# Kernel optimization log

Hardware: AMD Instinct MI355X
Metric: run time of the kernel (lower is better)

The kernel has to match this reference:

```python
import jax, jax.numpy as jnp
import numpy as np

END_INDEX = 0
MAX_STEPS = 20
BEAM = 5
K = 5  # per_node_beam_size
VN = -1e20
B, S, V, H, D = 32, 4, 20000, 512, 2048


def setup_inputs() -> dict:
    key = jax.random.key(0)
    ks = jax.random.split(key, 7)
    image_feature = jax.random.normal(ks[0], (B, D), jnp.float32)
    start_predictions = jax.random.randint(ks[1], (B,), 0, V)
    state_transform = jax.random.bernoulli(ks[2], 0.9, (B, S, S, V))
    emb = jax.random.normal(ks[3], (V, H), jnp.float32) * 0.02
    W_h = jax.random.normal(ks[4], (H, H), jnp.float32) * 0.02
    W_im = jax.random.normal(ks[5], (D, H), jnp.float32) * 0.02
    W_out = jax.random.normal(ks[6], (H, V), jnp.float32) * 0.02
    return dict(image_feature=image_feature, start_predictions=start_predictions,
                state_transform=state_transform, emb=emb, W_h=W_h, W_im=W_im, W_out=W_out)


def _step(image_feat, tokens, h, emb, W_h, W_im, W_out):
    # minimal recurrent decoder standing in for the injected step_func
    h_new = jnp.tanh(emb[tokens] + h @ W_h + image_feat @ W_im)
    log_probs = jax.nn.log_softmax(h_new @ W_out, axis=-1)
    return log_probs, h_new


def reference(image_feature, start_predictions, state_transform, emb, W_h, W_im, W_out):
    mask_t = jnp.swapaxes(state_transform, 1, 2)  # [B, S_tgt, S_src, V]
    h0 = jnp.zeros((B, H), jnp.float32)
    lp0, h = _step(image_feature, start_predictions, h0, emb, W_h, W_im, W_out)  # [B,V]
    # initial masked topk from init_state=0: transitions 0 -> s
    state_pred = jnp.where(state_transform[:, 0], lp0[:, None, :], VN)  # [B,S,V]
    last_lp, pred0 = jax.lax.top_k(state_pred, BEAM)  # [B,S,BEAM]
    pred0_flat = pred0.reshape(B, S * BEAM)

    def enlarge(t):  # [B, ...] -> [B*S*BEAM, ...]
        return jnp.broadcast_to(t[:, None, None], (B, S, BEAM) + t.shape[1:]).reshape((B * S * BEAM,) + t.shape[1:])

    h = enlarge(h)
    img = enlarge(image_feature)
    after_end = jnp.full((V,), VN, jnp.float32).at[END_INDEX].set(0.0)

    def scan_step(carry, _):
        h, last_preds, last_lp = carry
        lp, h_new = _step(img, last_preds.reshape(-1), h, emb, W_h, W_im, W_out)  # [N,V]
        cleaned = jnp.where((last_preds.reshape(-1) == END_INDEX)[:, None], after_end, lp)
        cleaned = cleaned.reshape(B, S, BEAM, V)
        # masked scores over all target states at once: [B, S_tgt, S_src, BEAM, V]
        masked = jnp.where(mask_t[:, :, :, None, :], cleaned[:, None], VN)
        top_lp, top_cls = jax.lax.top_k(masked, K)  # [B,St,Ss,BEAM,K]
        summed = top_lp + last_lp[:, None, :, :, None]
        flat_lp = summed.reshape(B, S, S * BEAM * K)
        flat_cls = top_cls.reshape(B, S, S * BEAM * K)
        beam_lp, beam_idx = jax.lax.top_k(flat_lp, BEAM)  # [B,St,BEAM]
        pred = jnp.take_along_axis(flat_cls, beam_idx, axis=2)
        bp = (beam_idx // K).reshape(B, S * BEAM)  # backpointer into S_src*BEAM
        h_nxt = jnp.take_along_axis(h_new.reshape(B, S * BEAM, H), bp[:, :, None], axis=1).reshape(B * S * BEAM, H)
        preds_flat = pred.reshape(B, S * BEAM)
        return (h_nxt, preds_flat, beam_lp), (preds_flat, bp)

    (_, _, last_lp), (preds_seq, bps) = jax.lax.scan(
        scan_step, (h, pred0_flat, last_lp), None, length=MAX_STEPS - 1)
    predictions = jnp.concatenate([pred0_flat[None], preds_seq], 0)  # [T, B, S*BEAM]

    # backtrack through backpointers (reverse scan over time)
    def back_step(cur_bp, inp):
        preds_t, bp_prev = inp
        rec = jnp.take_along_axis(preds_t, cur_bp, axis=1)
        return jnp.take_along_axis(bp_prev, cur_bp, axis=1), rec

    cur_bp, rec_mid = jax.lax.scan(back_step, bps[-1], (predictions[1:-1], bps[:-1]), reverse=True)
    rec0 = jnp.take_along_axis(predictions[0], cur_bp, axis=1)
    all_preds = jnp.concatenate([rec0[None], rec_mid, predictions[-1][None]], 0)  # [T,B,S*BEAM]
    all_predictions = jnp.moveaxis(all_preds, 0, 2).reshape(B, S, BEAM, MAX_STEPS)
    # select_state_func is user-injected; identity selection: return beams + scores
    return all_predictions, last_lp
```

## Files before the change

### kernel.cpp

```cpp
#include <hip/hip_runtime.h>
#include <hip/hip_bf16.h>
#include <stdint.h>
#include <stddef.h>

namespace {

constexpr int CB = 32;
constexpr int CS = 4;
constexpr int CV = 20000;
constexpr int CH = 512;
constexpr int CBEAM = 5;
constexpr int CT = 20;
constexpr int CNR = CB * CS * CBEAM;
constexpr int CSB = CS * CBEAM;
constexpr int CNM = CB * CS * CS * CV;
constexpr int CNP = CB * CS * CV;
constexpr float VNF = -1e20f;
constexpr float NEGINF = -3.402823466e+38f;
constexpr int IMAX = 0x7fffffff;

__global__ void detect_mode_k(const unsigned int* __restrict__ w, int* __restrict__ mode) {
  if (threadIdx.x != 0 || blockIdx.x != 0) return;
  int all01 = 1, odd1 = 0, f1 = 0;
  for (int i = 0; i < 256; ++i) {
    unsigned int x = w[i];
    if (x > 1u) all01 = 0;
    if ((i & 1) && x == 1u) odd1++;
    if (x == 0x3f800000u) f1++;
  }
  int md;
  if (f1 > 128) md = 3;
  else if (all01) md = (odd1 > 8) ? 1 : 2;
  else md = 0;
  *mode = md;
}

__global__ void convert_pack_k(const void* __restrict__ st, unsigned char* __restrict__ pm,
                               const int* __restrict__ mode) {
  int md = *mode;
  for (int i = blockIdx.x * blockDim.x + threadIdx.x; i < CNP; i += gridDim.x * blockDim.x) {
    int v = i % CV;
    int bs = i / CV;
    size_t base = (size_t)bs * 4 * CV + v;
    unsigned char r = 0;
#pragma unroll
    for (int s = 0; s < 4; ++s) {
      size_t idx = base + (size_t)s * CV;
      unsigned char bit;
      if (md == 0)      bit = ((const unsigned char*)st)[idx] != 0;
      else if (md == 1) bit = ((const unsigned int*)st)[idx] != 0;
      else if (md == 2) bit = ((const unsigned int*)st)[2 * idx] != 0;
      else              bit = (((const unsigned int*)st)[idx] & 0x7fffffffu) != 0;
      r |= (unsigned char)(bit << s);
    }
    pm[i] = r;
  }
}

__global__ __launch_bounds__(256) void img_proj_k(const float* __restrict__ img,
                                                  const float* __restrict__ Wim,
                                                  float* __restrict__ out) {
  int b = blockIdx.x, tid = threadIdx.x;
  __shared__ float simg[2048];
  for (int i = tid; i < 2048; i += 256) simg[i] = img[b * 2048 + i];
  __syncthreads();
  int c0 = tid * 2;
  float a0 = 0.f, a1 = 0.f;
  for (int k = 0; k < 2048; ++k) {
    float x = simg[k];
    float2 w = *(const float2*)&Wim[(size_t)k * CH + c0];
    a0 = fmaf(x, w.x, a0);
    a1 = fmaf(x, w.y, a1);
  }
  out[b * CH + c0] = a0;
  out[b * CH + c0 + 1] = a1;
}

__global__ void init_h_k(const float* __restrict__ emb, const int* __restrict__ start,
                         const float* __restrict__ imgp, float* __restrict__ H0) {
  int b = blockIdx.x, tid = threadIdx.x;
  int tok = start[b];
  for (int c = tid; c < CH; c += 256)
    H0[b * CH + c] = tanhf(emb[(size_t)tok * CH + c] + imgp[b * CH + c]);
}

template <int BM, int BN, int KB, int MT, int NT, int EPI>
__global__ __launch_bounds__(256) void gemm_k(
    const float* __restrict__ A, const int* __restrict__ rowmap,
    const float* __restrict__ Bm, float* __restrict__ C,
    int M, int N, int K,
    const int* __restrict__ tok, const float* __restrict__ emb,
    const float* __restrict__ imgp) {
  constexpr int TX = BN / NT;
  constexpr int TY = BM / MT;
  static_assert(TX * TY == 256, "thread count");
  static_assert((BM * KB / 4) % 256 == 0 && (KB * BN / 4) % 256 == 0, "stage");
  __shared__ float As[KB][BM + 4];
  __shared__ float Bs[KB][BN + 4];
  const int bm = blockIdx.y * BM;
  const int bn = blockIdx.x * BN;
  const int tid = threadIdx.x;
  const int tx = tid % TX, ty = tid / TX;
  float acc[MT][NT];
#pragma unroll
  for (int i = 0; i < MT; ++i)
#pragma unroll
    for (int j = 0; j < NT; ++j) acc[i][j] = 0.f;

  for (int k0 = 0; k0 < K; k0 += KB) {
    constexpr int AIT = BM * KB / 4 / 256;
#pragma unroll
    for (int it = 0; it < AIT; ++it) {
      int i = tid + it * 256;
      int r = i / (KB / 4);
      int kq = i % (KB / 4);
      int row = bm + r;
      float4 v = make_float4(0.f, 0.f, 0.f, 0.f);
      if (row < M) {
        int sr = rowmap ? rowmap[row] : row;
        v = *(const float4*)&A[(size_t)sr * K + k0 + kq * 4];
      }
      As[kq * 4 + 0][r] = v.x;
      As[kq * 4 + 1][r] = v.y;
      As[kq * 4 + 2][r] = v.z;
      As[kq * 4 + 3][r] = v.w;
    }
    constexpr int BIT = KB * BN / 4 / 256;
#pragma unroll
    for (int it = 0; it < BIT; ++it) {
      int i = tid + it * 256;
      int kk = i / (BN / 4);
      int cq = i % (BN / 4);
      int col = bn + cq * 4;
      float4 v = make_float4(0.f, 0.f, 0.f, 0.f);
      if (col < N) v = *(const float4*)&Bm[(size_t)(k0 + kk) * N + col];
      *(float4*)&Bs[kk][cq * 4] = v;
    }
    __syncthreads();
#pragma unroll 8
    for (int kk = 0; kk < KB; ++kk) {
      float a[MT], bb[NT];
#pragma unroll
      for (int i = 0; i < MT; ++i) a[i] = As[kk][ty * MT + i];
#pragma unroll
      for (int j = 0; j < NT; ++j) bb[j] = Bs[kk][tx * NT + j];
#pragma unroll
      for (int i = 0; i < MT; ++i)
#pragma unroll
        for (int j = 0; j < NT; ++j) acc[i][j] = fmaf(a[i], bb[j], acc[i][j]);
    }
    __syncthreads();
  }
#pragma unroll
  for (int i = 0; i < MT; ++i) {
    int row = bm + ty * MT + i;
    if (row < M) {
#pragma unroll
      for (int j4 = 0; j4 < NT / 4; ++j4) {
        int col = bn + tx * NT + j4 * 4;
        if (col < N) {
          float4 v;
          v.x = acc[i][j4 * 4 + 0];
          v.y = acc[i][j4 * 4 + 1];
          v.z = acc[i][j4 * 4 + 2];
          v.w = acc[i][j4 * 4 + 3];
          if (EPI == 1) {
            size_t eb = (size_t)tok[row] * N;
            int ib = (row / CSB) * N;
            v.x = tanhf(v.x + emb[eb + col + 0] + imgp[ib + col + 0]);
            v.y = tanhf(v.y + emb[eb + col + 1] + imgp[ib + col + 1]);
            v.z = tanhf(v.z + emb[eb + col + 2] + imgp[ib + col + 2]);
            v.w = tanhf(v.w + emb[eb + col + 3] + imgp[ib + col + 3]);
          }
          *(float4*)&C[(size_t)row * N + col] = v;
        }
      }
    }
  }
}

__global__ __launch_bounds__(256) void lse_k(const float* __restrict__ logits,
                                             float* __restrict__ lse) {
  int row = blockIdx.x;
  int tid = threadIdx.x;
  const float* lp = logits + (size_t)row * CV;
  __shared__ float red[4];
  float m = NEGINF;
  for (int v = tid * 4; v < CV; v += 1024) {
    float4 x = *(const float4*)(lp + v);
    m = fmaxf(m, fmaxf(fmaxf(x.x, x.y), fmaxf(x.z, x.w)));
  }
#pragma unroll
  for (int off = 32; off > 0; off >>= 1) m = fmaxf(m, __shfl_xor(m, off));
  if ((tid & 63) == 0) red[tid >> 6] = m;
  __syncthreads();
  m = fmaxf(fmaxf(red[0], red[1]), fmaxf(red[2], red[3]));
  __syncthreads();
  float s = 0.f;
  for (int v = tid * 4; v < CV; v += 1024) {
    float4 x = *(const float4*)(lp + v);
    s += expf(x.x - m) + expf(x.y - m) + expf(x.z - m) + expf(x.w - m);
  }
#pragma unroll
  for (int off = 32; off > 0; off >>= 1) s += __shfl_xor(s, off);
  if ((tid & 63) == 0) red[tid >> 6] = s;
  __syncthreads();
  if (tid == 0) lse[row] = m + logf(red[0] + red[1] + red[2] + red[3]);
}

struct L5 {
  float v0, v1, v2, v3, v4;
  int i0, i1, i2, i3, i4;
};

__device__ __forceinline__ void initL(L5& l) {
  l.v0 = l.v1 = l.v2 = l.v3 = l.v4 = NEGINF;
  l.i0 = l.i1 = l.i2 = l.i3 = l.i4 = IMAX;
}

__device__ __forceinline__ void insL(L5& l, float val, int idx) {
  if (!(val > l.v4)) return;
  if (val > l.v0) {
    l.v4 = l.v3; l.i4 = l.i3; l.v3 = l.v2; l.i3 = l.i2; l.v2 = l.v1; l.i2 = l.i1;
    l.v1 = l.v0; l.i1 = l.i0; l.v0 = val; l.i0 = idx;
  } else if (val > l.v1) {
    l.v4 = l.v3; l.i4 = l.i3; l.v3 = l.v2; l.i3 = l.i2; l.v2 = l.v1; l.i2 = l.i1;
    l.v1 = val; l.i1 = idx;
  } else if (val > l.v2) {
    l.v4 = l.v3; l.i4 = l.i3; l.v3 = l.v2; l.i3 = l.i2; l.v2 = val; l.i2 = idx;
  } else if (val > l.v3) {
    l.v4 = l.v3; l.i4 = l.i3; l.v3 = val; l.i3 = idx;
  } else {
    l.v4 = val; l.i4 = idx;
  }
}

__device__ __forceinline__ void mergeL(L5& A, L5 B) {
  float o0, o1, o2, o3, o4;
  int q0, q1, q2, q3, q4;
#define MSTEP(OV, OI)                                                                    \
  {                                                                                      \
    bool ta = (A.v0 > B.v0) || (A.v0 == B.v0 && A.i0 < B.i0);                            \
    if (ta) {                                                                            \
      OV = A.v0; OI = A.i0;                                                              \
      A.v0 = A.v1; A.i0 = A.i1; A.v1 = A.v2; A.i1 = A.i2; A.v2 = A.v3; A.i2 = A.i3;      \
      A.v3 = A.v4; A.i3 = A.i4; A.v4 = NEGINF; A.i4 = IMAX;                              \
    } else {                                                                             \
      OV = B.v0; OI = B.i0;                                                              \
      B.v0 = B.v1; B.i0 = B.i1; B.v1 = B.v2; B.i1 = B.i2; B.v2 = B.v3; B.i2 = B.i3;      \
      B.v3 = B.v4; B.i3 = B.i4; B.v4 = NEGINF; B.i4 = IMAX;                              \
    }                                                                                    \
  }
  MSTEP(o0, q0) MSTEP(o1, q1) MSTEP(o2, q2) MSTEP(o3, q3) MSTEP(o4, q4)
#undef MSTEP
  A.v0 = o0; A.v1 = o1; A.v2 = o2; A.v3 = o3; A.v4 = o4;
  A.i0 = q0; A.i1 = q1; A.i2 = q2; A.i3 = q3; A.i4 = q4;
}

__device__ __forceinline__ L5 shflxL(const L5& a, int off) {
  L5 r;
  r.v0 = __shfl_xor(a.v0, off); r.v1 = __shfl_xor(a.v1, off); r.v2 = __shfl_xor(a.v2, off);
  r.v3 = __shfl_xor(a.v3, off); r.v4 = __shfl_xor(a.v4, off);
  r.i0 = __shfl_xor(a.i0, off); r.i1 = __shfl_xor(a.i1, off); r.i2 = __shfl_xor(a.i2, off);
  r.i3 = __shfl_xor(a.i3, off); r.i4 = __shfl_xor(a.i4, off);
  return r;
}

template <bool INIT>
__global__ __launch_bounds__(256) void topk_half_k(
    const float* __restrict__ logits, const float* __restrict__ lse,
    const unsigned char* __restrict__ pmask, const int* __restrict__ last_preds,
    float* __restrict__ hv_lp, int* __restrict__ hv_cls) {
  constexpr int HV = CV / 2;
  constexpr int NG = HV / 4;
  int blk = blockIdx.x;
  int half = blk & 1, row = blk >> 1;
  int b, ss;
  if (INIT) { b = row; ss = 0; }
  else { b = row / CSB; ss = (row / CBEAM) % CS; }
  const int tid = threadIdx.x;
  const unsigned char* prow = pmask + (size_t)(b * CS + ss) * CV;

  if (!INIT && last_preds[row] == 0) {
    if (tid == 0) {
      unsigned char m0 = prow[0];
#pragma unroll
      for (int st = 0; st < 4; ++st) {
        int base = ((row * 4 + st) * 2 + half) * 5;
        if (half == 0) {
          hv_lp[base] = ((m0 >> st) & 1) ? 0.0f : VNF;
          hv_cls[base] = 0;
#pragma unroll
          for (int k = 1; k < 5; ++k) { hv_lp[base + k] = VNF; hv_cls[base + k] = k; }
        } else {
#pragma unroll
          for (int k = 0; k < 5; ++k) { hv_lp[base + k] = VNF; hv_cls[base + k] = HV + k; }
        }
      }
    }
    return;
  }

  const float* lprow = logits + (size_t)row * CV + (size_t)half * HV;
  const unsigned char* ph = prow + (size_t)half * HV;
  float lsev = lse[row];

  L5 lst0, lst1, lst2, lst3;
  initL(lst0); initL(lst1); initL(lst2); initL(lst3);

#define PROC1(VAL, IDX, BITS)                 \
  {                                           \
    if ((BITS) & 1) insL(lst0, VAL, IDX);     \
    if ((BITS) & 2) insL(lst1, VAL, IDX);     \
    if ((BITS) & 4) insL(lst2, VAL, IDX);     \
    if ((BITS) & 8) insL(lst3, VAL, IDX);     \
  }
#define PROC4(X, M, G)                                                        \
  {                                                                           \
    int ibase = half * HV + (G) * 4;                                          \
    float s0 = (X).x - lsev, s1 = (X).y - lsev;                               \
    float s2 = (X).z - lsev, s3 = (X).w - lsev;                               \
    PROC1(s0, ibase + 0, (M))                                                 \
    PROC1(s1, ibase + 1, (M) >> 8)                                            \
    PROC1(s2, ibase + 2, (M) >> 16)                                           \
    PROC1(s3, ibase + 3, (M) >> 24)                                           \
  }

  for (int g = tid; g < NG; g += 512) {
    int g2 = g + 256;
    float4 x0 = *(const float4*)(lprow + (size_t)g * 4);
    unsigned int m0 = *(const unsigned int*)(ph + (size_t)g * 4);
    float4 x1 = make_float4(0.f, 0.f, 0.f, 0.f);
    unsigned int m1 = 0;
    bool has1 = (g2 < NG);
    if (has1) {
      x1 = *(const float4*)(lprow + (size_t)g2 * 4);
      m1 = *(const unsigned int*)(ph + (size_t)g2 * 4);
    }
    PROC4(x0, m0, g)
    if (has1) PROC4(x1, m1, g2)
  }
#undef PROC4
#undef PROC1

#pragma unroll
  for (int off = 1; off < 64; off <<= 1) {
    mergeL(lst0, shflxL(lst0, off));
    mergeL(lst1, shflxL(lst1, off));
    mergeL(lst2, shflxL(lst2, off));
    mergeL(lst3, shflxL(lst3, off));
  }

  __shared__ float swv[4][4][5];
  __shared__ int swi[4][4][5];
  int wid = tid >> 6, lane = tid & 63;
  if (lane == 0) {
#define POST(L, ST)                                                     \
    swv[wid][ST][0] = L.v0; swv[wid][ST][1] = L.v1; swv[wid][ST][2] = L.v2; \
    swv[wid][ST][3] = L.v3; swv[wid][ST][4] = L.v4;                     \
    swi[wid][ST][0] = L.i0; swi[wid][ST][1] = L.i1; swi[wid][ST][2] = L.i2; \
    swi[wid][ST][3] = L.i3; swi[wid][ST][4] = L.i4;
    POST(lst0, 0) POST(lst1, 1) POST(lst2, 2) POST(lst3, 3)
#undef POST
  }
  __syncthreads();
  if (tid == 0) {
#pragma unroll
    for (int st = 0; st < 4; ++st) {
      L5 A;
      A.v0 = swv[0][st][0]; A.v1 = swv[0][st][1]; A.v2 = swv[0][st][2];
      A.v3 = swv[0][st][3]; A.v4 = swv[0][st][4];
      A.i0 = swi[0][st][0]; A.i1 = swi[0][st][1]; A.i2 = swi[0][st][2];
      A.i3 = swi[0][st][3]; A.i4 = swi[0][st][4];
#pragma unroll
      for (int w = 1; w < 4; ++w) {
        L5 Bb;
        Bb.v0 = swv[w][st][0]; Bb.v1 = swv[w][st][1]; Bb.v2 = swv[w][st][2];
        Bb.v3 = swv[w][st][3]; Bb.v4 = swv[w][st][4];
        Bb.i0 = swi[w][st][0]; Bb.i1 = swi[w][st][1]; Bb.i2 = swi[w][st][2];
        Bb.i3 = swi[w][st][3]; Bb.i4 = swi[w][st][4];
        mergeL(A, Bb);
      }
      int base = ((row * 4 + st) * 2 + half) * 5;
      hv_lp[base + 0] = A.v0; hv_lp[base + 1] = A.v1; hv_lp[base + 2] = A.v2;
      hv_lp[base + 3] = A.v3; hv_lp[base + 4] = A.v4;
      hv_cls[base + 0] = A.i0; hv_cls[base + 1] = A.i1; hv_cls[base + 2] = A.i2;
      hv_cls[base + 3] = A.i3; hv_cls[base + 4] = A.i4;
    }
  }
}

template <bool INIT>
__global__ void merge_halves_k(const float* __restrict__ hv_lp, const int* __restrict__ hv_cls,
                               float* __restrict__ top_lp, int* __restrict__ top_cls,
                               float* __restrict__ lp0, int* __restrict__ preds0,
                               int* __restrict__ lastp_out, int* __restrict__ rowmap) {
  int gid = blockIdx.x * blockDim.x + threadIdx.x;
  int nit = (INIT ? CB : CNR) * 4;
  if (gid >= nit) return;
  int row = gid / 4, st = gid % 4;
  const float* a = hv_lp + (size_t)gid * 10;
  const int* ai = hv_cls + (size_t)gid * 10;
  L5 A, Bb;
  A.v0 = a[0]; A.v1 = a[1]; A.v2 = a[2]; A.v3 = a[3]; A.v4 = a[4];
  A.i0 = ai[0]; A.i1 = ai[1]; A.i2 = ai[2]; A.i3 = ai[3]; A.i4 = ai[4];
  Bb.v0 = a[5]; Bb.v1 = a[6]; Bb.v2 = a[7]; Bb.v3 = a[8]; Bb.v4 = a[9];
  Bb.i0 = ai[5]; Bb.i1 = ai[6]; Bb.i2 = ai[7]; Bb.i3 = ai[8]; Bb.i4 = ai[9];
  mergeL(A, Bb);
  if (INIT) {
    int slot = row * CSB + st * 5;
    float vv[5] = {A.v0, A.v1, A.v2, A.v3, A.v4};
    int ii[5] = {A.i0, A.i1, A.i2, A.i3, A.i4};
#pragma unroll
    for (int k = 0; k < 5; ++k) {
      lp0[slot + k] = vv[k];
      preds0[slot + k] = ii[k];
      lastp_out[slot + k] = ii[k];
      rowmap[slot + k] = row;
    }
  } else {
    int b = row / CSB, ss = (row / CBEAM) % CS, beam = row % CBEAM;
    int o = (((b * CS + st) * CS + ss) * CBEAM + beam) * 5;
    top_lp[o + 0] = A.v0; top_lp[o + 1] = A.v1; top_lp[o + 2] = A.v2;
    top_lp[o + 3] = A.v3; top_lp[o + 4] = A.v4;
    top_cls[o + 0] = A.i0; top_cls[o + 1] = A.i1; top_cls[o + 2] = A.i2;
    top_cls[o + 3] = A.i3; top_cls[o + 4] = A.i4;
  }
}

__global__ __launch_bounds__(128) void beam_sel_k(
    const float* __restrict__ top_lp, const int* __restrict__ top_cls,
    const float* __restrict__ lp_old, float* __restrict__ lp_new,
    int* __restrict__ last_preds, int* __restrict__ rowmap,
    int* __restrict__ preds_t, int* __restrict__ bps_t) {
  int b = blockIdx.x / CS, st = blockIdx.x % CS;
  int tid = threadIdx.x;
  __shared__ float sv[128];
  __shared__ int si[128];
  float val = NEGINF;
  int idx = IMAX;
  if (tid < 100) {
    int ss = tid / 25, rem = tid % 25;
    int beam = rem / 5, k = rem % 5;
    val = top_lp[(size_t)(((b * CS + st) * CS + ss) * CBEAM + beam) * 5 + k] +
          lp_old[(b * CS + ss) * CBEAM + beam];
    idx = tid;
  }
  for (int r = 0; r < 5; ++r) {
    sv[tid] = val;
    si[tid] = idx;
    __syncthreads();
    for (int off = 64; off > 0; off >>= 1) {
      if (tid < off) {
        float w = sv[tid + off];
        int wi = si[tid + off];
        if (w > sv[tid] || (w == sv[tid] && wi < si[tid])) { sv[tid] = w; si[tid] = wi; }
      }
      __syncthreads();
    }
    float wval = sv[0];
    int widx = si[0];
    if (idx == widx) { val = NEGINF; idx = IMAX; }
    if (tid == r) {
      int ss = widx / 25, rem = widx % 25;
      int beam = rem / 5, k = rem % 5;
      int pred = top_cls[(size_t)(((b * CS + st) * CS + ss) * CBEAM + beam) * 5 + k];
      int bp = widx / 5;
      int slot = (b * CS + st) * CBEAM + r;
      lp_new[slot] = wval;
      preds_t[slot] = pred;
      bps_t[slot] = bp;
      last_preds[slot] = pred;
      rowmap[slot] = b * CSB + bp;
    }
    __syncthreads();
  }
}

__global__ void backtrack_k(const int* __restrict__ preds, const int* __restrict__ bps,
                            const float* __restrict__ lpfin, float* __restrict__ out) {
  int b = blockIdx.x, j = threadIdx.x;
  if (j >= CSB) return;
  int s = j / CBEAM, bm = j % CBEAM;
  int obase = ((b * CS + s) * CBEAM + bm) * CT;
  int tok = preds[(CT - 1) * CNR + b * CSB + j];
  out[obase + CT - 1] = (float)tok;
  int cur = bps[(CT - 2) * CNR + b * CSB + j];
  for (int t = CT - 2; t >= 1; --t) {
    tok = preds[t * CNR + b * CSB + cur];
    out[obase + t] = (float)tok;
    cur = bps[(t - 1) * CNR + b * CSB + cur];
  }
  tok = preds[0 * CNR + b * CSB + cur];
  out[obase + 0] = (float)tok;
  out[CB * CS * CBEAM * CT + b * CSB + j] = lpfin[b * CSB + j];
}

}

extern "C" void kernel_launch(void* const* d_in, const int* in_sizes, int n_in,
                              void* d_out, int out_size, void* d_ws, size_t ws_size,
                              hipStream_t stream) {
  (void)in_sizes; (void)n_in; (void)out_size; (void)ws_size;
  const float* img = (const float*)d_in[0];
  const int* startp = (const int*)d_in[1];
  const void* straw = d_in[2];
  const float* emb = (const float*)d_in[3];
  const float* Wh = (const float*)d_in[4];
  const float* Wim = (const float*)d_in[5];
  const float* Wout = (const float*)d_in[6];
  float* out = (float*)d_out;

  char* ws = (char*)d_ws;
  size_t off = 0;
  auto take = [&](size_t bytes) -> char* {
    char* p = ws + off;
    off += (bytes + 255) & ~(size_t)255;
    return p;
  };
  unsigned char* pmask = (unsigned char*)take((size_t)CNP);
  int* modep = (int*)take(256);
  float* imgproj = (float*)take((size_t)CB * CH * 4);
  float* H0 = (float*)take((size_t)CNR * CH * 4);
  float* H1 = (float*)take((size_t)CNR * CH * 4);
  float* logits = (float*)take((size_t)CNR * CV * 4);
  float* lsebuf = (float*)take((size_t)CNR * 4);
  float* LP0 = (float*)take((size_t)CNR * 4);
  float* LP1 = (float*)take((size_t)CNR * 4);
  int* lastp = (int*)take((size_t)CNR * 4);
  int* rowmap = (int*)take((size_t)CNR * 4);
  float* toplp = (float*)take((size_t)2560 * 5 * 4);
  int* topcls = (int*)take((size_t)2560 * 5 * 4);
  float* hvlp = (float*)take((size_t)CNR * 4 * 2 * 5 * 4);
  int* hvcls = (int*)take((size_t)CNR * 4 * 2 * 5 * 4);
  int* predsq = (int*)take((size_t)CT * CNR * 4);
  int* bpsq = (int*)take((size_t)(CT - 1) * CNR * 4);

  detect_mode_k<<<1, 64, 0, stream>>>((const unsigned int*)straw, modep);
  convert_pack_k<<<1024, 256, 0, stream>>>(straw, pmask, modep);
  img_proj_k<<<CB, 256, 0, stream>>>(img, Wim, imgproj);
  init_h_k<<<CB, 256, 0, stream>>>(emb, startp, imgproj, H0);
  gemm_k<128, 128, 32, 8, 8, 0><<<dim3(157, 1), 256, 0, stream>>>(
      H0, nullptr, Wout, logits, CB, CV, CH, nullptr, nullptr, nullptr);
  lse_k<<<CB, 256, 0, stream>>>(logits, lsebuf);
  topk_half_k<true><<<CB * 2, 256, 0, stream>>>(logits, lsebuf, pmask, nullptr, hvlp, hvcls);
  merge_halves_k<true><<<1, 128, 0, stream>>>(hvlp, hvcls, nullptr, nullptr, LP0, predsq,
                                              lastp, rowmap);
  for (int t = 1; t < CT; ++t) {
    float* hprev = (t & 1) ? H0 : H1;
    float* hcur = (t & 1) ? H1 : H0;
    float* lpold = (t & 1) ? LP0 : LP1;
    float* lpnew = (t & 1) ? LP1 : LP0;
    gemm_k<32, 64, 32, 2, 4, 1><<<dim3(8, 20), 256, 0, stream>>>(
        hprev, rowmap, Wh, hcur, CNR, CH, CH, lastp, emb, imgproj);
    gemm_k<128, 128, 32, 8, 8, 0><<<dim3(157, 5), 256, 0, stream>>>(
        hcur, nullptr, Wout, logits, CNR, CV, CH, nullptr, nullptr, nullptr);
    lse_k<<<CNR, 256, 0, stream>>>(logits, lsebuf);
    topk_half_k<false><<<CNR * 2, 256, 0, stream>>>(logits, lsebuf, pmask, lastp, hvlp, hvcls);
    merge_halves_k<false><<<10, 256, 0, stream>>>(hvlp, hvcls, toplp, topcls, nullptr,
                                                  nullptr, nullptr, nullptr);
    beam_sel_k<<<CB * CS, 128, 0, stream>>>(toplp, topcls, lpold, lpnew, lastp, rowmap,
                                            predsq + (size_t)t * CNR,
                                            bpsq + (size_t)(t - 1) * CNR);
  }
  backtrack_k<<<CB, 32, 0, stream>>>(predsq, bpsq, LP1, out);
}
```

Before: 6.675 ms.

## Fuse output GEMM with log-softmax and masked top-k using split-fp16 MFMA

Replaces the fp32 SIMT output projection, the separate log-sum-exp pass and the top-k passes with one fused kernel per step. It uses fp16 matrix-core instructions with a hi/lo split of both operands (three MFMAs per tile) to approximate fp32 accuracy. Each tile computes partial online max/sum and a masked top-5 per state in registers, so the full 640x20000 logits matrix is never written to or reread from global memory. A small reduce kernel then merges the per-tile partials. The costs are a one-time transpose and split of W_out, scaled split arithmetic that could perturb ties and ordering, and more partial-merge work.

```diff
diff --git a/kernel.cpp b/kernel.cpp
--- a/kernel.cpp
+++ b/kernel.cpp
@@ -5,19 +5,31 @@
 
 namespace {
 
+typedef _Float16 f16;
+typedef __attribute__((ext_vector_type(8))) _Float16 f16x8;
+typedef __attribute__((ext_vector_type(4))) _Float16 f16x4;
+typedef __attribute__((ext_vector_type(4))) float f32x4;
+
 constexpr int CB = 32;
 constexpr int CS = 4;
 constexpr int CV = 20000;
+constexpr int CVP = 20224;
+constexpr int NTILE = 79;
 constexpr int CH = 512;
 constexpr int CBEAM = 5;
 constexpr int CT = 20;
 constexpr int CNR = CB * CS * CBEAM;
 constexpr int CSB = CS * CBEAM;
-constexpr int CNM = CB * CS * CS * CV;
 constexpr int CNP = CB * CS * CV;
 constexpr float VNF = -1e20f;
 constexpr float NEGINF = -3.402823466e+38f;
 constexpr int IMAX = 0x7fffffff;
+
+__device__ __forceinline__ void f2h2(float x, f16& h, f16& l) {
+  float xs = x * 256.0f;
+  h = (f16)xs;
+  l = (f16)(xs - (float)h);
+}
 
 __global__ void detect_mode_k(const unsigned int* __restrict__ w, int* __restrict__ mode) {
   if (threadIdx.x != 0 || blockIdx.x != 0) return;
@@ -54,6 +66,32 @@
       r |= (unsigned char)(bit << s);
     }
     pm[i] = r;
+  }
+}
+
+__global__ __launch_bounds__(256) void conv_wout_k(const float* __restrict__ W,
+                                                   f16* __restrict__ BTh,
+                                                   f16* __restrict__ BTl) {
+  __shared__ float t[64][65];
+  int n0 = blockIdx.x * 64, k0 = blockIdx.y * 64;
+  int tid = threadIdx.x;
+  int c = tid & 63, r4 = tid >> 6;
+#pragma unroll
+  for (int i = 0; i < 16; ++i) {
+    int kr = r4 + i * 4;
+    int n = n0 + c;
+    t[kr][c] = (n < CV) ? W[(size_t)(k0 + kr) * CV + n] : 0.f;
+  }
+  __syncthreads();
+#pragma unroll
+  for (int i = 0; i < 16; ++i) {
+    int nr = r4 + i * 4;
+    float x = t[c][nr];
+    f16 h, l;
+    f2h2(x, h, l);
+    size_t o = (size_t)(n0 + nr) * CH + k0 + c;
+    BTh[o] = h;
+    BTl[o] = l;
   }
 }
 
@@ -77,24 +115,30 @@
 }
 
 __global__ void init_h_k(const float* __restrict__ emb, const int* __restrict__ start,
-                         const float* __restrict__ imgp, float* __restrict__ H0) {
+                         const float* __restrict__ imgp, float* __restrict__ H0,
+                         f16* __restrict__ Hh, f16* __restrict__ Hl) {
   int b = blockIdx.x, tid = threadIdx.x;
   int tok = start[b];
-  for (int c = tid; c < CH; c += 256)
-    H0[b * CH + c] = tanhf(emb[(size_t)tok * CH + c] + imgp[b * CH + c]);
-}
-
-template <int BM, int BN, int KB, int MT, int NT, int EPI>
+  for (int c = tid; c < CH; c += 256) {
+    float v = tanhf(emb[(size_t)tok * CH + c] + imgp[b * CH + c]);
+    H0[b * CH + c] = v;
+    f16 h, l;
+    f2h2(v, h, l);
+    Hh[b * CH + c] = h;
+    Hl[b * CH + c] = l;
+  }
+}
+
+template <int BM, int BN, int KB, int MT, int NT>
 __global__ __launch_bounds__(256) void gemm_k(
     const float* __restrict__ A, const int* __restrict__ rowmap,
     const float* __restrict__ Bm, float* __restrict__ C,
     int M, int N, int K,
     const int* __restrict__ tok, const float* __restrict__ emb,
-    const float* __restrict__ imgp) {
+    const float* __restrict__ imgp, f16* __restrict__ Hh, f16* __restrict__ Hl) {
   constexpr int TX = BN / NT;
   constexpr int TY = BM / MT;
   static_assert(TX * TY == 256, "thread count");
-  static_assert((BM * KB / 4) % 256 == 0 && (KB * BN / 4) % 256 == 0, "stage");
   __shared__ float As[KB][BM + 4];
   __shared__ float Bs[KB][BN + 4];
   const int bm = blockIdx.y * BM;
@@ -164,48 +208,26 @@
           v.y = acc[i][j4 * 4 + 1];
           v.z = acc[i][j4 * 4 + 2];
           v.w = acc[i][j4 * 4 + 3];
-          if (EPI == 1) {
-            size_t eb = (size_t)tok[row] * N;
-            int ib = (row / CSB) * N;
-            v.x = tanhf(v.x + emb[eb + col + 0] + imgp[ib + col + 0]);
-            v.y = tanhf(v.y + emb[eb + col + 1] + imgp[ib + col + 1]);
-            v.z = tanhf(v.z + emb[eb + col + 2] + imgp[ib + col + 2]);
-            v.w = tanhf(v.w + emb[eb + col + 3] + imgp[ib + col + 3]);
-          }
+          size_t eb = (size_t)tok[row] * N;
+          int ib = (row / CSB) * N;
+          v.x = tanhf(v.x + emb[eb + col + 0] + imgp[ib + col + 0]);
+          v.y = tanhf(v.y + emb[eb + col + 1] + imgp[ib + col + 1]);
+          v.z = tanhf(v.z + emb[eb + col + 2] + imgp[ib + col + 2]);
+          v.w = tanhf(v.w + emb[eb + col + 3] + imgp[ib + col + 3]);
           *(float4*)&C[(size_t)row * N + col] = v;
+          f16 h0, h1, h2, h3, l0, l1, l2, l3;
+          f2h2(v.x, h0, l0);
+          f2h2(v.y, h1, l1);
+          f2h2(v.z, h2, l2);
+          f2h2(v.w, h3, l3);
+          f16x4 hv = {h0, h1, h2, h3};
+          f16x4 lv = {l0, l1, l2, l3};
+          *(f16x4*)&Hh[(size_t)row * N + col] = hv;
+          *(f16x4*)&Hl[(size_t)row * N + col] = lv;
         }
       }
     }
   }
-}
-
-__global__ __launch_bounds__(256) void lse_k(const float* __restrict__ logits,
-                                             float* __restrict__ lse) {
-  int row = blockIdx.x;
-  int tid = threadIdx.x;
-  const float* lp = logits + (size_t)row * CV;
-  __shared__ float red[4];
-  float m = NEGINF;
-  for (int v = tid * 4; v < CV; v += 1024) {
-    float4 x = *(const float4*)(lp + v);
-    m = fmaxf(m, fmaxf(fmaxf(x.x, x.y), fmaxf(x.z, x.w)));
-  }
-#pragma unroll
-  for (int off = 32; off > 0; off >>= 1) m = fmaxf(m, __shfl_xor(m, off));
-  if ((tid & 63) == 0) red[tid >> 6] = m;
-  __syncthreads();
-  m = fmaxf(fmaxf(red[0], red[1]), fmaxf(red[2], red[3]));
-  __syncthreads();
-  float s = 0.f;
-  for (int v = tid * 4; v < CV; v += 1024) {
-    float4 x = *(const float4*)(lp + v);
-    s += expf(x.x - m) + expf(x.y - m) + expf(x.z - m) + expf(x.w - m);
-  }
-#pragma unroll
-  for (int off = 32; off > 0; off >>= 1) s += __shfl_xor(s, off);
-  if ((tid & 63) == 0) red[tid >> 6] = s;
-  __syncthreads();
-  if (tid == 0) lse[row] = m + logf(red[0] + red[1] + red[2] + red[3]);
 }
 
 struct L5 {
@@ -267,169 +289,261 @@
 }
 
 template <bool INIT>
-__global__ __launch_bounds__(256) void topk_half_k(
-    const float* __restrict__ logits, const float* __restrict__ lse,
-    const unsigned char* __restrict__ pmask, const int* __restrict__ last_preds,
-    float* __restrict__ hv_lp, int* __restrict__ hv_cls) {
-  constexpr int HV = CV / 2;
-  constexpr int NG = HV / 4;
-  int blk = blockIdx.x;
-  int half = blk & 1, row = blk >> 1;
-  int b, ss;
-  if (INIT) { b = row; ss = 0; }
-  else { b = row / CSB; ss = (row / CBEAM) % CS; }
+__global__ __launch_bounds__(256) void fused_gemm_k(
+    const f16* __restrict__ Ah, const f16* __restrict__ Al,
+    const f16* __restrict__ BTh, const f16* __restrict__ BTl,
+    const unsigned char* __restrict__ pmask,
+    float* __restrict__ pv, unsigned short* __restrict__ pi, float* __restrict__ pms) {
+  const int tile = blockIdx.x;
+  const int bty = blockIdx.y * 64;
   const int tid = threadIdx.x;
-  const unsigned char* prow = pmask + (size_t)(b * CS + ss) * CV;
-
-  if (!INIT && last_preds[row] == 0) {
-    if (tid == 0) {
-      unsigned char m0 = prow[0];
-#pragma unroll
-      for (int st = 0; st < 4; ++st) {
-        int base = ((row * 4 + st) * 2 + half) * 5;
-        if (half == 0) {
-          hv_lp[base] = ((m0 >> st) & 1) ? 0.0f : VNF;
-          hv_cls[base] = 0;
-#pragma unroll
-          for (int k = 1; k < 5; ++k) { hv_lp[base + k] = VNF; hv_cls[base + k] = k; }
-        } else {
-#pragma unroll
-          for (int k = 0; k < 5; ++k) { hv_lp[base + k] = VNF; hv_cls[base + k] = HV + k; }
+  const int w = tid >> 6;
+  const int lane = tid & 63;
+  const int l16 = lane & 15, lq = lane >> 4;
+  const int vwave = tile * 256 + w * 64;
+
+  const f16* pvh = BTh + (size_t)(vwave + l16) * CH + lq * 8;
+  const f16* pvl = BTl + (size_t)(vwave + l16) * CH + lq * 8;
+  const f16* pbh = Ah + (size_t)(bty + l16) * CH + lq * 8;
+  const f16* pbl = Al + (size_t)(bty + l16) * CH + lq * 8;
+
+  f32x4 acc[4][4] = {};
+  for (int k0 = 0; k0 < CH; k0 += 32) {
+    f16x8 vh[4], vl[4], bh[4], bl[4];
+#pragma unroll
+    for (int i = 0; i < 4; ++i) {
+      vh[i] = *(const f16x8*)(pvh + (size_t)i * 16 * CH + k0);
+      vl[i] = *(const f16x8*)(pvl + (size_t)i * 16 * CH + k0);
+      bh[i] = *(const f16x8*)(pbh + (size_t)i * 16 * CH + k0);
+      bl[i] = *(const f16x8*)(pbl + (size_t)i * 16 * CH + k0);
+    }
+#pragma unroll
+    for (int vf = 0; vf < 4; ++vf)
+#pragma unroll
+      for (int bt = 0; bt < 4; ++bt) {
+        acc[vf][bt] = __builtin_amdgcn_mfma_f32_16x16x32_f16(vh[vf], bh[bt], acc[vf][bt], 0, 0, 0);
+        acc[vf][bt] = __builtin_amdgcn_mfma_f32_16x16x32_f16(vh[vf], bl[bt], acc[vf][bt], 0, 0, 0);
+        acc[vf][bt] = __builtin_amdgcn_mfma_f32_16x16x32_f16(vl[vf], bh[bt], acc[vf][bt], 0, 0, 0);
+      }
+  }
+
+  __shared__ float lv[4][64][4][5];
+  __shared__ unsigned short li[4][64][4][5];
+  __shared__ float lms[4][64][2];
+
+#pragma unroll
+  for (int bt = 0; bt < 4; ++bt) {
+    const int btrow = bty + bt * 16 + l16;
+    int mrow;
+    if (INIT) mrow = min(btrow, CB - 1) * CS;
+    else {
+      int b = btrow / CSB;
+      int ss = (btrow % CSB) / CBEAM;
+      mrow = b * CS + ss;
+    }
+    const unsigned char* pmrow = pmask + (size_t)mrow * CV;
+    float xv[4][4];
+    unsigned int msk[4];
+    float mloc = NEGINF;
+#pragma unroll
+    for (int vf = 0; vf < 4; ++vf) {
+      int cb = vwave + vf * 16 + lq * 4;
+      msk[vf] = *(const unsigned int*)(pmrow + cb);
+#pragma unroll
+      for (int rr = 0; rr < 4; ++rr) {
+        float x = acc[vf][bt][rr] * (1.0f / 65536.0f);
+        bool ok = (cb + rr) < CV;
+        xv[vf][rr] = ok ? x : NEGINF;
+        if (ok) mloc = fmaxf(mloc, x);
+      }
+    }
+    float sloc = 0.f;
+    L5 ls0, ls1, ls2, ls3;
+    initL(ls0); initL(ls1); initL(ls2); initL(ls3);
+#pragma unroll
+    for (int vf = 0; vf < 4; ++vf) {
+      int cb = vwave + vf * 16 + lq * 4;
+#pragma unroll
+      for (int rr = 0; rr < 4; ++rr) {
+        int col = cb + rr;
+        if (col < CV) {
+          float x = xv[vf][rr];
+          sloc += expf(x - mloc);
+          unsigned int bits = msk[vf] >> (rr * 8);
+          if (bits & 1u) insL(ls0, x, col);
+          if (bits & 2u) insL(ls1, x, col);
+          if (bits & 4u) insL(ls2, x, col);
+          if (bits & 8u) insL(ls3, x, col);
         }
       }
     }
-    return;
-  }
-
-  const float* lprow = logits + (size_t)row * CV + (size_t)half * HV;
-  const unsigned char* ph = prow + (size_t)half * HV;
-  float lsev = lse[row];
-
-  L5 lst0, lst1, lst2, lst3;
-  initL(lst0); initL(lst1); initL(lst2); initL(lst3);
-
-#define PROC1(VAL, IDX, BITS)                 \
-  {                                           \
-    if ((BITS) & 1) insL(lst0, VAL, IDX);     \
-    if ((BITS) & 2) insL(lst1, VAL, IDX);     \
-    if ((BITS) & 4) insL(lst2, VAL, IDX);     \
-    if ((BITS) & 8) insL(lst3, VAL, IDX);     \
-  }
-#define PROC4(X, M, G)                                                        \
-  {                                                                           \
-    int ibase = half * HV + (G) * 4;                                          \
-    float s0 = (X).x - lsev, s1 = (X).y - lsev;                               \
-    float s2 = (X).z - lsev, s3 = (X).w - lsev;                               \
-    PROC1(s0, ibase + 0, (M))                                                 \
-    PROC1(s1, ibase + 1, (M) >> 8)                                            \
-    PROC1(s2, ibase + 2, (M) >> 16)                                           \
-    PROC1(s3, ibase + 3, (M) >> 24)                                           \
-  }
-
-  for (int g = tid; g < NG; g += 512) {
-    int g2 = g + 256;
-    float4 x0 = *(const float4*)(lprow + (size_t)g * 4);
-    unsigned int m0 = *(const unsigned int*)(ph + (size_t)g * 4);
-    float4 x1 = make_float4(0.f, 0.f, 0.f, 0.f);
-    unsigned int m1 = 0;
-    bool has1 = (g2 < NG);
-    if (has1) {
-      x1 = *(const float4*)(lprow + (size_t)g2 * 4);
-      m1 = *(const unsigned int*)(ph + (size_t)g2 * 4);
-    }
-    PROC4(x0, m0, g)
-    if (has1) PROC4(x1, m1, g2)
-  }
-#undef PROC4
-#undef PROC1
-
-#pragma unroll
-  for (int off = 1; off < 64; off <<= 1) {
-    mergeL(lst0, shflxL(lst0, off));
-    mergeL(lst1, shflxL(lst1, off));
-    mergeL(lst2, shflxL(lst2, off));
-    mergeL(lst3, shflxL(lst3, off));
-  }
-
-  __shared__ float swv[4][4][5];
-  __shared__ int swi[4][4][5];
-  int wid = tid >> 6, lane = tid & 63;
-  if (lane == 0) {
-#define POST(L, ST)                                                     \
-    swv[wid][ST][0] = L.v0; swv[wid][ST][1] = L.v1; swv[wid][ST][2] = L.v2; \
-    swv[wid][ST][3] = L.v3; swv[wid][ST][4] = L.v4;                     \
-    swi[wid][ST][0] = L.i0; swi[wid][ST][1] = L.i1; swi[wid][ST][2] = L.i2; \
-    swi[wid][ST][3] = L.i3; swi[wid][ST][4] = L.i4;
-    POST(lst0, 0) POST(lst1, 1) POST(lst2, 2) POST(lst3, 3)
-#undef POST
+#pragma unroll
+    for (int off = 16; off <= 32; off <<= 1) {
+      mergeL(ls0, shflxL(ls0, off));
+      mergeL(ls1, shflxL(ls1, off));
+      mergeL(ls2, shflxL(ls2, off));
+      mergeL(ls3, shflxL(ls3, off));
+      float m2 = __shfl_xor(mloc, off);
+      float s2 = __shfl_xor(sloc, off);
+      float mn = fmaxf(mloc, m2);
+      sloc = sloc * expf(mloc - mn) + s2 * expf(m2 - mn);
+      mloc = mn;
+    }
+    if (lq == 0) {
+      int lrow = bt * 16 + l16;
+#define PUT(L, ST)                                                                      \
+      lv[w][lrow][ST][0] = L.v0; lv[w][lrow][ST][1] = L.v1; lv[w][lrow][ST][2] = L.v2;  \
+      lv[w][lrow][ST][3] = L.v3; lv[w][lrow][ST][4] = L.v4;                             \
+      li[w][lrow][ST][0] = (unsigned short)L.i0; li[w][lrow][ST][1] = (unsigned short)L.i1; \
+      li[w][lrow][ST][2] = (unsigned short)L.i2; li[w][lrow][ST][3] = (unsigned short)L.i3; \
+      li[w][lrow][ST][4] = (unsigned short)L.i4;
+      PUT(ls0, 0) PUT(ls1, 1) PUT(ls2, 2) PUT(ls3, 3)
+#undef PUT
+      lms[w][lrow][0] = mloc;
+      lms[w][lrow][1] = sloc;
+    }
   }
   __syncthreads();
-  if (tid == 0) {
-#pragma unroll
-    for (int st = 0; st < 4; ++st) {
-      L5 A;
-      A.v0 = swv[0][st][0]; A.v1 = swv[0][st][1]; A.v2 = swv[0][st][2];
-      A.v3 = swv[0][st][3]; A.v4 = swv[0][st][4];
-      A.i0 = swi[0][st][0]; A.i1 = swi[0][st][1]; A.i2 = swi[0][st][2];
-      A.i3 = swi[0][st][3]; A.i4 = swi[0][st][4];
-#pragma unroll
-      for (int w = 1; w < 4; ++w) {
-        L5 Bb;
-        Bb.v0 = swv[w][st][0]; Bb.v1 = swv[w][st][1]; Bb.v2 = swv[w][st][2];
-        Bb.v3 = swv[w][st][3]; Bb.v4 = swv[w][st][4];
-        Bb.i0 = swi[w][st][0]; Bb.i1 = swi[w][st][1]; Bb.i2 = swi[w][st][2];
-        Bb.i3 = swi[w][st][3]; Bb.i4 = swi[w][st][4];
-        mergeL(A, Bb);
-      }
-      int base = ((row * 4 + st) * 2 + half) * 5;
-      hv_lp[base + 0] = A.v0; hv_lp[base + 1] = A.v1; hv_lp[base + 2] = A.v2;
-      hv_lp[base + 3] = A.v3; hv_lp[base + 4] = A.v4;
-      hv_cls[base + 0] = A.i0; hv_cls[base + 1] = A.i1; hv_cls[base + 2] = A.i2;
-      hv_cls[base + 3] = A.i3; hv_cls[base + 4] = A.i4;
+
+  {
+    int row64 = tid >> 2, st = tid & 3;
+    L5 A;
+    A.v0 = lv[0][row64][st][0]; A.v1 = lv[0][row64][st][1]; A.v2 = lv[0][row64][st][2];
+    A.v3 = lv[0][row64][st][3]; A.v4 = lv[0][row64][st][4];
+    A.i0 = li[0][row64][st][0]; A.i1 = li[0][row64][st][1]; A.i2 = li[0][row64][st][2];
+    A.i3 = li[0][row64][st][3]; A.i4 = li[0][row64][st][4];
+#pragma unroll
+    for (int ww = 1; ww < 4; ++ww) {
+      L5 B;
+      B.v0 = lv[ww][row64][st][0]; B.v1 = lv[ww][row64][st][1]; B.v2 = lv[ww][row64][st][2];
+      B.v3 = lv[ww][row64][st][3]; B.v4 = lv[ww][row64][st][4];
+      B.i0 = li[ww][row64][st][0]; B.i1 = li[ww][row64][st][1]; B.i2 = li[ww][row64][st][2];
+      B.i3 = li[ww][row64][st][3]; B.i4 = li[ww][row64][st][4];
+      mergeL(A, B);
+    }
+    int grow = bty + row64;
+    size_t pbase = ((size_t)tile * CNR + grow) * 20 + st * 5;
+    pv[pbase + 0] = A.v0; pv[pbase + 1] = A.v1; pv[pbase + 2] = A.v2;
+    pv[pbase + 3] = A.v3; pv[pbase + 4] = A.v4;
+    pi[pbase + 0] = (unsigned short)A.i0; pi[pbase + 1] = (unsigned short)A.i1;
+    pi[pbase + 2] = (unsigned short)A.i2; pi[pbase + 3] = (unsigned short)A.i3;
+    pi[pbase + 4] = (unsigned short)A.i4;
+    if (st == 0) {
+      float m = lms[0][row64][0], s = lms[0][row64][1];
+#pragma unroll
+      for (int ww = 1; ww < 4; ++ww) {
+        float m2 = lms[ww][row64][0], s2 = lms[ww][row64][1];
+        float mn = fmaxf(m, m2);
+        s = s * expf(m - mn) + s2 * expf(m2 - mn);
+        m = mn;
+      }
+      pms[((size_t)tile * CNR + grow) * 2 + 0] = m;
+      pms[((size_t)tile * CNR + grow) * 2 + 1] = s;
     }
   }
 }
 
 template <bool INIT>
-__global__ void merge_halves_k(const float* __restrict__ hv_lp, const int* __restrict__ hv_cls,
-                               float* __restrict__ top_lp, int* __restrict__ top_cls,
-                               float* __restrict__ lp0, int* __restrict__ preds0,
-                               int* __restrict__ lastp_out, int* __restrict__ rowmap) {
-  int gid = blockIdx.x * blockDim.x + threadIdx.x;
-  int nit = (INIT ? CB : CNR) * 4;
-  if (gid >= nit) return;
-  int row = gid / 4, st = gid % 4;
-  const float* a = hv_lp + (size_t)gid * 10;
-  const int* ai = hv_cls + (size_t)gid * 10;
-  L5 A, Bb;
-  A.v0 = a[0]; A.v1 = a[1]; A.v2 = a[2]; A.v3 = a[3]; A.v4 = a[4];
-  A.i0 = ai[0]; A.i1 = ai[1]; A.i2 = ai[2]; A.i3 = ai[3]; A.i4 = ai[4];
-  Bb.v0 = a[5]; Bb.v1 = a[6]; Bb.v2 = a[7]; Bb.v3 = a[8]; Bb.v4 = a[9];
-  Bb.i0 = ai[5]; Bb.i1 = ai[6]; Bb.i2 = ai[7]; Bb.i3 = ai[8]; Bb.i4 = ai[9];
-  mergeL(A, Bb);
-  if (INIT) {
-    int slot = row * CSB + st * 5;
-    float vv[5] = {A.v0, A.v1, A.v2, A.v3, A.v4};
-    int ii[5] = {A.i0, A.i1, A.i2, A.i3, A.i4};
-#pragma unroll
-    for (int k = 0; k < 5; ++k) {
-      lp0[slot + k] = vv[k];
-      preds0[slot + k] = ii[k];
-      lastp_out[slot + k] = ii[k];
-      rowmap[slot + k] = row;
-    }
-  } else {
-    int b = row / CSB, ss = (row / CBEAM) % CS, beam = row % CBEAM;
-    int o = (((b * CS + st) * CS + ss) * CBEAM + beam) * 5;
-    top_lp[o + 0] = A.v0; top_lp[o + 1] = A.v1; top_lp[o + 2] = A.v2;
-    top_lp[o + 3] = A.v3; top_lp[o + 4] = A.v4;
-    top_cls[o + 0] = A.i0; top_cls[o + 1] = A.i1; top_cls[o + 2] = A.i2;
-    top_cls[o + 3] = A.i3; top_cls[o + 4] = A.i4;
+__global__ __launch_bounds__(64) void reduce_k(
+    const float* __restrict__ pv, const unsigned short* __restrict__ pi,
+    const float* __restrict__ pms, const unsigned char* __restrict__ pmask,
+    const int* __restrict__ lastp_in,
+    float* __restrict__ fin_v, int* __restrict__ fin_i, float* __restrict__ lsebuf,
+    float* __restrict__ lp0, int* __restrict__ preds0,
+    int* __restrict__ lastp_out, int* __restrict__ rowmap) {
+  int row = blockIdx.x;
+  int t = threadIdx.x;
+  int st = t >> 4, c = t & 15;
+  L5 A;
+  initL(A);
+  float m = NEGINF, s = 0.f;
+  for (int j = 0; j < 5; ++j) {
+    int tl = c * 5 + j;
+    if (tl >= NTILE) break;
+    size_t base = ((size_t)tl * CNR + row) * 20 + st * 5;
+    L5 B;
+    B.v0 = pv[base + 0]; B.v1 = pv[base + 1]; B.v2 = pv[base + 2];
+    B.v3 = pv[base + 3]; B.v4 = pv[base + 4];
+    B.i0 = pi[base + 0]; B.i1 = pi[base + 1]; B.i2 = pi[base + 2];
+    B.i3 = pi[base + 3]; B.i4 = pi[base + 4];
+    mergeL(A, B);
+    if (st == 0) {
+      float mt = pms[((size_t)tl * CNR + row) * 2 + 0];
+      float stv = pms[((size_t)tl * CNR + row) * 2 + 1];
+      float mn = fmaxf(m, mt);
+      s = s * expf(m - mn) + stv * expf(mt - mn);
+      m = mn;
+    }
+  }
+  __shared__ float shv[4][16][5];
+  __shared__ int shi[4][16][5];
+  __shared__ float shm[16], shs[16];
+  __shared__ float shlse;
+  shv[st][c][0] = A.v0; shv[st][c][1] = A.v1; shv[st][c][2] = A.v2;
+  shv[st][c][3] = A.v3; shv[st][c][4] = A.v4;
+  shi[st][c][0] = A.i0; shi[st][c][1] = A.i1; shi[st][c][2] = A.i2;
+  shi[st][c][3] = A.i3; shi[st][c][4] = A.i4;
+  if (st == 0) { shm[c] = m; shs[c] = s; }
+  for (int off = 8; off >= 1; off >>= 1) {
+    __syncthreads();
+    if (c < off) {
+      L5 B;
+      B.v0 = shv[st][c + off][0]; B.v1 = shv[st][c + off][1]; B.v2 = shv[st][c + off][2];
+      B.v3 = shv[st][c + off][3]; B.v4 = shv[st][c + off][4];
+      B.i0 = shi[st][c + off][0]; B.i1 = shi[st][c + off][1]; B.i2 = shi[st][c + off][2];
+      B.i3 = shi[st][c + off][3]; B.i4 = shi[st][c + off][4];
+      mergeL(A, B);
+      shv[st][c][0] = A.v0; shv[st][c][1] = A.v1; shv[st][c][2] = A.v2;
+      shv[st][c][3] = A.v3; shv[st][c][4] = A.v4;
+      shi[st][c][0] = A.i0; shi[st][c][1] = A.i1; shi[st][c][2] = A.i2;
+      shi[st][c][3] = A.i3; shi[st][c][4] = A.i4;
+      if (st == 0) {
+        float m2 = shm[c + off], s2 = shs[c + off];
+        float mn = fmaxf(m, m2);
+        s = s * expf(m - mn) + s2 * expf(m2 - mn);
+        m = mn;
+        shm[c] = m; shs[c] = s;
+      }
+    }
+  }
+  __syncthreads();
+  if (t == 0) shlse = shm[0] + logf(shs[0]);
+  __syncthreads();
+  float lse = shlse;
+  if (c == 0) {
+    if (INIT) {
+      float vv[5] = {A.v0, A.v1, A.v2, A.v3, A.v4};
+      int ii[5] = {A.i0, A.i1, A.i2, A.i3, A.i4};
+      int slot = row * CSB + st * 5;
+#pragma unroll
+      for (int k = 0; k < 5; ++k) {
+        lp0[slot + k] = vv[k] - lse;
+        preds0[slot + k] = ii[k];
+        lastp_out[slot + k] = ii[k];
+        rowmap[slot + k] = row;
+      }
+    } else {
+      bool ended = (lastp_in[row] == 0);
+      if (ended) {
+        int b = row / CSB, ss = (row % CSB) / CBEAM;
+        unsigned char mb = pmask[(size_t)(b * CS + ss) * CV];
+        A.v0 = ((mb >> st) & 1) ? 0.0f : VNF; A.i0 = 0;
+        A.v1 = VNF; A.i1 = 1; A.v2 = VNF; A.i2 = 2;
+        A.v3 = VNF; A.i3 = 3; A.v4 = VNF; A.i4 = 4;
+      }
+      size_t fb = ((size_t)row * 4 + st) * 5;
+      fin_v[fb + 0] = A.v0; fin_v[fb + 1] = A.v1; fin_v[fb + 2] = A.v2;
+      fin_v[fb + 3] = A.v3; fin_v[fb + 4] = A.v4;
+      fin_i[fb + 0] = A.i0; fin_i[fb + 1] = A.i1; fin_i[fb + 2] = A.i2;
+      fin_i[fb + 3] = A.i3; fin_i[fb + 4] = A.i4;
+      if (st == 0) lsebuf[row] = ended ? 0.f : lse;
+    }
   }
 }
 
 __global__ __launch_bounds__(128) void beam_sel_k(
-    const float* __restrict__ top_lp, const int* __restrict__ top_cls,
+    const float* __restrict__ fin_v, const int* __restrict__ fin_i,
+    const float* __restrict__ lsebuf,
     const float* __restrict__ lp_old, float* __restrict__ lp_new,
     int* __restrict__ last_preds, int* __restrict__ rowmap,
     int* __restrict__ preds_t, int* __restrict__ bps_t) {
@@ -440,10 +554,9 @@
   float val = NEGINF;
   int idx = IMAX;
   if (tid < 100) {
-    int ss = tid / 25, rem = tid % 25;
-    int beam = rem / 5, k = rem % 5;
-    val = top_lp[(size_t)(((b * CS + st) * CS + ss) * CBEAM + beam) * 5 + k] +
-          lp_old[(b * CS + ss) * CBEAM + beam];
+    int r5 = tid / 5, k = tid % 5;
+    int row = b * CSB + r5;
+    val = fin_v[((size_t)row * 4 + st) * 5 + k] - lsebuf[row] + lp_old[row];
     idx = tid;
   }
   for (int r = 0; r < 5; ++r) {
@@ -462,10 +575,10 @@
     int widx = si[0];
     if (idx == widx) { val = NEGINF; idx = IMAX; }
     if (tid == r) {
-      int ss = widx / 25, rem = widx % 25;
-      int beam = rem / 5, k = rem % 5;
-      int pred = top_cls[(size_t)(((b * CS + st) * CS + ss) * CBEAM + beam) * 5 + k];
-      int bp = widx / 5;
+      int r5 = widx / 5, k = widx % 5;
+      int row = b * CSB + r5;
+      int pred = fin_i[((size_t)row * 4 + st) * 5 + k];
+      int bp = r5;
       int slot = (b * CS + st) * CBEAM + r;
       lp_new[slot] = wval;
       preds_t[slot] = pred;
@@ -518,48 +631,48 @@
     off += (bytes + 255) & ~(size_t)255;
     return p;
   };
-  unsigned char* pmask = (unsigned char*)take((size_t)CNP);
+  unsigned char* pmask = (unsigned char*)take((size_t)CNP + 512);
   int* modep = (int*)take(256);
   float* imgproj = (float*)take((size_t)CB * CH * 4);
   float* H0 = (float*)take((size_t)CNR * CH * 4);
   float* H1 = (float*)take((size_t)CNR * CH * 4);
-  float* logits = (float*)take((size_t)CNR * CV * 4);
   float* lsebuf = (float*)take((size_t)CNR * 4);
   float* LP0 = (float*)take((size_t)CNR * 4);
   float* LP1 = (float*)take((size_t)CNR * 4);
   int* lastp = (int*)take((size_t)CNR * 4);
   int* rowmap = (int*)take((size_t)CNR * 4);
-  float* toplp = (float*)take((size_t)2560 * 5 * 4);
-  int* topcls = (int*)take((size_t)2560 * 5 * 4);
-  float* hvlp = (float*)take((size_t)CNR * 4 * 2 * 5 * 4);
-  int* hvcls = (int*)take((size_t)CNR * 4 * 2 * 5 * 4);
   int* predsq = (int*)take((size_t)CT * CNR * 4);
   int* bpsq = (int*)take((size_t)(CT - 1) * CNR * 4);
+  f16* BTh = (f16*)take((size_t)CVP * CH * 2);
+  f16* BTl = (f16*)take((size_t)CVP * CH * 2);
+  f16* Hh = (f16*)take((size_t)CNR * CH * 2);
+  f16* Hl = (f16*)take((size_t)CNR * CH * 2);
+  float* pv = (float*)take((size_t)NTILE * CNR * 20 * 4);
+  unsigned short* pi = (unsigned short*)take((size_t)NTILE * CNR * 20 * 2);
+  float* pms = (float*)take((size_t)NTILE * CNR * 2 * 4);
+  float* finv = (float*)take((size_t)CNR * 4 * 5 * 4);
+  int* fini = (int*)take((size_t)CNR * 4 * 5 * 4);
 
   detect_mode_k<<<1, 64, 0, stream>>>((const unsigned int*)straw, modep);
   convert_pack_k<<<1024, 256, 0, stream>>>(straw, pmask, modep);
+  conv_wout_k<<<dim3(CVP / 64, CH / 64), 256, 0, stream>>>(Wout, BTh, BTl);
   img_proj_k<<<CB, 256, 0, stream>>>(img, Wim, imgproj);
-  init_h_k<<<CB, 256, 0, stream>>>(emb, startp, imgproj, H0);
-  gemm_k<128, 128, 32, 8, 8, 0><<<dim3(157, 1), 256, 0, stream>>>(
-      H0, nullptr, Wout, logits, CB, CV, CH, nullptr, nullptr, nullptr);
-  lse_k<<<CB, 256, 0, stream>>>(logits, lsebuf);
-  topk_half_k<true><<<CB * 2, 256, 0, stream>>>(logits, lsebuf, pmask, nullptr, hvlp, hvcls);
-  merge_halves_k<true><<<1, 128, 0, stream>>>(hvlp, hvcls, nullptr, nullptr, LP0, predsq,
-                                              lastp, rowmap);
+  init_h_k<<<CB, 256, 0, stream>>>(emb, startp, imgproj, H0, Hh, Hl);
+
+  fused_gemm_k<true><<<dim3(NTILE, 1), 256, 0, stream>>>(Hh, Hl, BTh, BTl, pmask, pv, pi, pms);
+  reduce_k<true><<<CB, 64, 0, stream>>>(pv, pi, pms, pmask, nullptr, nullptr, nullptr,
+                                        nullptr, LP0, predsq, lastp, rowmap);
   for (int t = 1; t < CT; ++t) {
     float* hprev = (t & 1) ? H0 : H1;
     float* hcur = (t & 1) ? H1 : H0;
     float* lpold = (t & 1) ? LP0 : LP1;
     float* lpnew = (t & 1) ? LP1 : LP0;
-    gemm_k<32, 64, 32, 2, 4, 1><<<dim3(8, 20), 256, 0, stream>>>(
-        hprev, rowmap, Wh, hcur, CNR, CH, CH, lastp, emb, imgproj);
-    gemm_k<128, 128, 32, 8, 8, 0><<<dim3(157, 5), 256, 0, stream>>>(
-        hcur, nullptr, Wout, logits, CNR, CV, CH, nullptr, nullptr, nullptr);
-    lse_k<<<CNR, 256, 0, stream>>>(logits, lsebuf);
-    topk_half_k<false><<<CNR * 2, 256, 0, stream>>>(logits, lsebuf, pmask, lastp, hvlp, hvcls);
-    merge_halves_k<false><<<10, 256, 0, stream>>>(hvlp, hvcls, toplp, topcls, nullptr,
-                                                  nullptr, nullptr, nullptr);
-    beam_sel_k<<<CB * CS, 128, 0, stream>>>(toplp, topcls, lpold, lpnew, lastp, rowmap,
+    gemm_k<32, 64, 32, 2, 4><<<dim3(8, 20), 256, 0, stream>>>(
+        hprev, rowmap, Wh, hcur, CNR, CH, CH, lastp, emb, imgproj, Hh, Hl);
+    fused_gemm_k<false><<<dim3(NTILE, 10), 256, 0, stream>>>(Hh, Hl, BTh, BTl, pmask, pv, pi, pms);
+    reduce_k<false><<<CNR, 64, 0, stream>>>(pv, pi, pms, pmask, lastp, finv, fini, lsebuf,
+                                            nullptr, nullptr, nullptr, nullptr);
+    beam_sel_k<<<CB * CS, 128, 0, stream>>>(finv, fini, lsebuf, lpold, lpnew, lastp, rowmap,
                                             predsq + (size_t)t * CNR,
                                             bpsq + (size_t)(t - 1) * CNR);
   }
```

After: 8.153 ms. 1.22x slower.
